# Kernel tuning notes

Hardware: AMD Instinct MI355X
Metric: run time of the kernel (lower is better)

Reference implementation:

```python
import jax, jax.numpy as jnp
from jax import lax
import numpy as np

B, T, H, NCLS = 64, 2048, 128, 4
CHANS = [1, 4, 8, 16, 96]


def setup_inputs() -> dict:
    key = jax.random.key(0)
    ks = iter(jax.random.split(key, 64))

    def n(shape, s=0.05):
        return jax.random.normal(next(ks), shape, jnp.float32) * s

    inp = {}
    inp["x"] = jax.random.normal(next(ks), (B, T, 1), jnp.float32)
    lengths = jnp.sort(jax.random.randint(next(ks), (B,), T // 2, T + 1))[::-1]
    inp["lengths"] = lengths.at[0].set(T).astype(jnp.int32)
    inp["ff_w"] = n((H, 1))
    inp["ff_b"] = n((H,))
    for l in range(2):
        din = H if l == 0 else 2 * H
        for d in ("f", "b"):
            inp[f"w_ih_l{l}{d}"] = n((4 * H, din))
            inp[f"w_hh_l{l}{d}"] = n((4 * H, H))
            inp[f"b_ih_l{l}{d}"] = n((4 * H,))
            inp[f"b_hh_l{l}{d}"] = n((4 * H,))
    for i in range(4):
        fan_in = CHANS[i] * 3
        inp[f"cw{i}"] = n((CHANS[i + 1], CHANS[i], 3), float(np.sqrt(2.0 / fan_in)))
        inp[f"cb{i}"] = n((CHANS[i + 1],))
    inp["lin_w"] = n((NCLS, 96 + 6 * H))
    inp["lin_b"] = n((NCLS,))
    return inp


def _lstm_scan(x, w_ih, w_hh, b_ih, b_hh):
    # x: [B, T, D] -> hidden states [B, T, H]; PyTorch gate order i,f,g,o
    b = x.shape[0]
    h0 = jnp.zeros((b, H), x.dtype)
    xg = jnp.swapaxes(x, 0, 1) @ w_ih.T + (b_ih + b_hh)  # [T, B, 4H] input contribution

    def step(carry, g_in):
        h, c = carry
        g = g_in + h @ w_hh.T
        i, f, gg, o = jnp.split(g, 4, axis=-1)
        c = jax.nn.sigmoid(f) * c + jax.nn.sigmoid(i) * jnp.tanh(gg)
        h = jax.nn.sigmoid(o) * jnp.tanh(c)
        return (h, c), h

    _, ys = lax.scan(step, (h0, h0), xg)
    return jnp.swapaxes(ys, 0, 1)


def _forward(x, lengths, ff_w, ff_b, lstm_params, conv_params, lin_w, lin_b):
    t = x.shape[1]
    mask = jnp.arange(t)[None, :] < lengths[:, None]            # [B, T]
    maskf = mask[..., None].astype(x.dtype)                      # [B, T, 1]
    # reversal index for packed-sequence-style backward direction (valid part reversed)
    rev_idx = jnp.clip(lengths[:, None] - 1 - jnp.arange(t)[None, :], 0, t - 1)[..., None]

    inp = (x @ ff_w.T + ff_b) * maskf                            # [B, T, H]
    for (wif, whf, bif, bhf, wib, whb, bib, bhb) in lstm_params:
        f_out = _lstm_scan(inp, wif, whf, bif, bhf)
        rin = jnp.take_along_axis(inp, rev_idx, axis=1) * maskf
        rys = _lstm_scan(rin, wib, whb, bib, bhb)
        b_out = jnp.take_along_axis(rys, rev_idx, axis=1)
        inp = jnp.concatenate([f_out, b_out], axis=-1) * maskf   # [B, T, 2H]

    rnn = inp
    lens = lengths.astype(x.dtype)[:, None]
    h_mean = (rnn * maskf).sum(1) / lens
    h_max = jnp.where(mask[..., None], rnn, -jnp.inf).max(1)
    h_last = jnp.take_along_axis(rnn, (lengths - 1)[:, None, None], axis=1)[:, 0]
    h = jnp.concatenate([h_mean, h_max, h_last], axis=1)         # [B, 6H]

    c = jnp.swapaxes(x, 1, 2)                                    # [B, 1, T]
    for cw, cb in conv_params:
        c = lax.conv_general_dilated(c, cw, (1,), 'VALID',
                                     dimension_numbers=('NCH', 'OIH', 'NCH'))
        c = jax.nn.relu(c + cb[None, :, None])
    cavg = c.mean(-1)                                            # [B, 96]

    out = jnp.concatenate([cavg, h], axis=1) @ lin_w.T + lin_b
    return out


def reference(x, lengths, ff_w, ff_b,
              w_ih_l0f, w_hh_l0f, b_ih_l0f, b_hh_l0f,
              w_ih_l0b, w_hh_l0b, b_ih_l0b, b_hh_l0b,
              w_ih_l1f, w_hh_l1f, b_ih_l1f, b_hh_l1f,
              w_ih_l1b, w_hh_l1b, b_ih_l1b, b_hh_l1b,
              cw0, cb0, cw1, cb1, cw2, cb2, cw3, cb3,
              lin_w, lin_b):
    lstm_params = [
        (w_ih_l0f, w_hh_l0f, b_ih_l0f, b_hh_l0f, w_ih_l0b, w_hh_l0b, b_ih_l0b, b_hh_l0b),
        (w_ih_l1f, w_hh_l1f, b_ih_l1f, b_hh_l1f, w_ih_l1b, w_hh_l1b, b_ih_l1b, b_hh_l1b),
    ]
    conv_params = [(cw0, cb0), (cw1, cb1), (cw2, cb2), (cw3, cb3)]
    return _forward(x, lengths, ff_w, ff_b, lstm_params, conv_params, lin_w, lin_b)
```

## Files before the change

### kernel.cpp

```cpp
#include <hip/hip_runtime.h>

using u16 = unsigned short;
using u32 = unsigned int;

typedef __attribute__((ext_vector_type(8))) short bf16x8;
typedef __attribute__((ext_vector_type(4))) float f32x4;

#define L2E 1.44269504f

__device__ __forceinline__ float bf2f(u16 u) {
  union { u32 i; float f; } v; v.i = ((u32)u) << 16; return v.f;
}
__device__ __forceinline__ u16 f2bf(float f) {
  union { float f; u32 i; } v; v.f = f;
  u32 i = v.i;
  return (u16)((i + 0x7FFFu + ((i >> 16) & 1u)) >> 16);
}
__device__ __forceinline__ float fexp2(float x) { float r; asm("v_exp_f32 %0, %1" : "=v"(r) : "v"(x)); return r; }
__device__ __forceinline__ float frcp(float x) { float r; asm("v_rcp_f32 %0, %1" : "=v"(r) : "v"(x)); return r; }
__device__ __forceinline__ float sig_s(float xp) { return frcp(1.0f + fexp2(-xp)); }
__device__ __forceinline__ float tanh_s(float x2) { return fmaf(-2.0f, frcp(1.0f + fexp2(x2)), 1.0f); }

__device__ __forceinline__ void barrier_lgkm() {
  asm volatile("s_waitcnt lgkmcnt(0)\n\ts_barrier" ::: "memory");
}

__device__ __forceinline__ float ldin(const void* p, long i, int f32) {
  return f32 ? ((const float*)p)[i] : bf2f(((const u16*)p)[i]);
}
__device__ __forceinline__ bf16x8 ldfrag(const void* p, long i, int f32) {
  if (!f32) return *(const bf16x8*)((const u16*)p + i);
  const float* f = (const float*)p + i;
  bf16x8 r;
#pragma unroll
  for (int j = 0; j < 8; ++j) r[j] = (short)f2bf(f[j]);
  return r;
}
__device__ __forceinline__ bf16x8 ldfrag_s(const void* p, long i, int f32, float s) {
  bf16x8 r;
  if (!f32) {
    const u16* h = (const u16*)p + i;
#pragma unroll
    for (int j = 0; j < 8; ++j) r[j] = (short)f2bf(bf2f(h[j]) * s);
  } else {
    const float* f = (const float*)p + i;
#pragma unroll
    for (int j = 0; j < 8; ++j) r[j] = (short)f2bf(f[j] * s);
  }
  return r;
}
__device__ __forceinline__ uint2 ld4(const void* p, long i, int f32) {
  if (!f32) return *(const uint2*)((const u16*)p + i);
  const float* f = (const float*)p + i;
  return make_uint2((u32)f2bf(f[0]) | ((u32)f2bf(f[1]) << 16),
                    (u32)f2bf(f[2]) | ((u32)f2bf(f[3]) << 16));
}

__device__ __forceinline__ int dtype_probe(const void* ffw) {
  const u16* h = (const u16*)ffw;
  int sane = 0;
  for (int i = 0; i < 64; ++i) {
    float v = bf2f(h[i]);
    sane += (v == v && fabsf(v) <= 1.0f) ? 1 : 0;
  }
  return (sane >= 60) ? 0 : 1;
}

__global__ void prep_k(const void* ffw, const void* ffb,
                       const void* wih0f, const void* bih0f, const void* bhh0f,
                       const void* wih0b, const void* bih0b, const void* bhh0b,
                       const void* bih1f, const void* bhh1f,
                       const void* bih1b, const void* bhh1b,
                       float* __restrict__ prep0, float* __restrict__ bias1) {
  const int f32 = dtype_probe(ffw);
  int dir = blockIdx.x, r = threadIdx.x;
  const void* wih  = dir ? wih0b : wih0f;
  const void* bih0 = dir ? bih0b : bih0f;
  const void* bhh0 = dir ? bhh0b : bhh0f;
  const void* bih1 = dir ? bih1b : bih1f;
  const void* bhh1 = dir ? bhh1b : bhh1f;
  float u = 0.f, v = 0.f;
  for (int k = 0; k < 128; ++k) {
    float wv = ldin(wih, r * 128 + k, f32);
    u += wv * ldin(ffw, k, f32);
    v += wv * ldin(ffb, k, f32);
  }
  const float sc = ((r >> 7) == 2) ? 2.0f * L2E : L2E;
  float bi = ldin(bih0, r, f32) + ldin(bhh0, r, f32);
  prep0[dir * 1536 + r]        = u * sc;
  prep0[dir * 1536 + 512 + r]  = (bi + v) * sc;
  prep0[dir * 1536 + 1024 + r] = bi * sc;
  bias1[dir * 512 + r] = (ldin(bih1, r, f32) + ldin(bhh1, r, f32)) * sc;
}

__device__ void conv_body(int blk, int tid, const void* x,
                          const void* cw0, const void* cb0, const void* cw1, const void* cb1,
                          const void* cw2, const void* cb2, const void* cw3, const void* cb3,
                          int f32, float* __restrict__ pcavg) {
  int b = blk >> 3, ck = blk & 7;
  int P = ck * 255;
  __shared__ float xs[264];
  __shared__ float c1s[4][264];
  __shared__ float c2s[8][264];
  __shared__ float w0s[12], w1s[96], w2s[384], w3s[4608];
  __shared__ float b0s[4], b1s[8], b2s[16], b3s[96];
  __shared__ float red[8][96];
  for (int i = tid; i < 263; i += 512) xs[i] = ldin(x, (long)b * 2048 + P + i, f32);
  for (int i = tid; i < 12; i += 512) w0s[i] = ldin(cw0, i, f32);
  for (int i = tid; i < 96; i += 512) w1s[i] = ldin(cw1, i, f32);
  for (int i = tid; i < 384; i += 512) w2s[i] = ldin(cw2, i, f32);
  for (int i = tid; i < 4608; i += 512) w3s[i] = ldin(cw3, i, f32);
  if (tid < 4) b0s[tid] = ldin(cb0, tid, f32);
  if (tid < 8) b1s[tid] = ldin(cb1, tid, f32);
  if (tid < 16) b2s[tid] = ldin(cb2, tid, f32);
  if (tid < 96) b3s[tid] = ldin(cb3, tid, f32);
  __syncthreads();
  for (int i = tid; i < 4 * 261; i += 512) {
    int ch = i / 261, t = i % 261;
    float s = b0s[ch];
#pragma unroll
    for (int d = 0; d < 3; ++d) s += w0s[ch * 3 + d] * xs[t + d];
    c1s[ch][t] = fmaxf(s, 0.f);
  }
  __syncthreads();
  for (int i = tid; i < 8 * 259; i += 512) {
    int ch = i / 259, t = i % 259;
    float s = b1s[ch];
    for (int ic = 0; ic < 4; ++ic)
#pragma unroll
      for (int d = 0; d < 3; ++d) s += w1s[(ch * 4 + ic) * 3 + d] * c1s[ic][t + d];
    c2s[ch][t] = fmaxf(s, 0.f);
  }
  __syncthreads();
  const bool act = tid < 255;
  float c3w[16][3];
#pragma unroll
  for (int m = 0; m < 16; ++m)
#pragma unroll
    for (int dt = 0; dt < 3; ++dt) c3w[m][dt] = 0.f;
  if (act) {
#pragma unroll
    for (int m = 0; m < 16; ++m)
#pragma unroll
      for (int dt = 0; dt < 3; ++dt) {
        float s = b2s[m];
        for (int ic = 0; ic < 8; ++ic)
#pragma unroll
          for (int d = 0; d < 3; ++d) s += w2s[(m * 8 + ic) * 3 + d] * c2s[ic][tid + dt + d];
        c3w[m][dt] = fmaxf(s, 0.f);
      }
  }
  int wv = tid >> 6, lane = tid & 63;
  for (int o = 0; o < 96; ++o) {
    float s = b3s[o];
#pragma unroll
    for (int m = 0; m < 16; ++m)
#pragma unroll
      for (int dt = 0; dt < 3; ++dt) s += w3s[(o * 16 + m) * 3 + dt] * c3w[m][dt];
    float v = act ? fmaxf(s, 0.f) : 0.f;
    for (int off = 32; off > 0; off >>= 1) v += __shfl_down(v, off, 64);
    if (lane == 0) red[wv][o] = v;
  }
  __syncthreads();
  if (tid < 96) {
    float s = 0.f;
#pragma unroll
    for (int k = 0; k < 8; ++k) s += red[k][tid];
    pcavg[(size_t)(b * 8 + ck) * 96 + tid] = s;
  }
}

__device__ void xg_gemm_body(int bi, int tid,
                             const void* wih1f, const void* wih1b,
                             const float* __restrict__ bias1,
                             const u16* __restrict__ f0, const u16* __restrict__ r0,
                             const int* __restrict__ lengths,
                             u16* __restrict__ xg_wr, int ct0, int tc, int f32) {
  const int TCB = 32;
  int nt = tc / TCB;
  int dir = bi / (4 * nt);
  int rem = bi % (4 * nt);
  int g = rem / nt, tcb = rem % nt;
  int tstart = ct0 + tcb * TCB;
  const int w = tid >> 6, lane = tid & 63, q = lane >> 4, col = lane & 15;

  const void* wih = dir ? wih1b : wih1f;
  bf16x8 af[4][8];
#pragma unroll
  for (int gt = 0; gt < 4; ++gt)
#pragma unroll
    for (int kt = 0; kt < 8; ++kt)
      af[gt][kt] = ldfrag(wih, (long)(gt * 128 + w * 16 + col) * 256 + kt * 32 + q * 8, f32);
  f32x4 bias4[4];
#pragma unroll
  for (int gt = 0; gt < 4; ++gt)
    bias4[gt] = *(const f32x4*)(bias1 + dir * 512 + gt * 128 + w * 16 + q * 4);

  __shared__ u16 bin[2][16][264];
  int sb = tid >> 5, sk = (tid & 31) * 8;
  int gb = g * 16 + sb;
  int len_s = lengths[gb];

  auto stage = [&](int t, int buf) {
    uint4 v = make_uint4(0u, 0u, 0u, 0u);
    if (t < len_s) {
      int qt = len_s - 1 - t; if (qt < 0) qt = 0;
      int th0 = dir ? qt : t;
      int th1 = dir ? t : qt;
      if (sk < 128)
        v = *(const uint4*)(f0 + ((size_t)th0 * 64 + gb) * 128 + sk);
      else
        v = *(const uint4*)(r0 + ((size_t)th1 * 64 + gb) * 128 + sk - 128);
    }
    *(uint4*)&bin[buf][sb][sk] = v;
  };
  stage(tstart, 0);
  const int bglob = g * 16 + col;
  const int G4o = bglob >> 2, c4g = bglob & 3;
  for (int i = 0; i < TCB; ++i) {
    int t = tstart + i, buf = i & 1;
    barrier_lgkm();
    if (i + 1 < TCB) stage(t + 1, buf ^ 1);
    bf16x8 bfr[8];
#pragma unroll
    for (int kt = 0; kt < 8; ++kt) bfr[kt] = *(const bf16x8*)(&bin[buf][col][kt * 32 + q * 8]);
    f32x4 acc[4];
#pragma unroll
    for (int gt = 0; gt < 4; ++gt) acc[gt] = (f32x4){0.f, 0.f, 0.f, 0.f};
#pragma unroll
    for (int kt = 0; kt < 8; ++kt)
#pragma unroll
      for (int gt = 0; gt < 4; ++gt)
        acc[gt] = __builtin_amdgcn_mfma_f32_16x16x32_bf16(af[gt][kt], bfr[kt], acc[gt], 0, 0, 0);
    size_t eb = ((((size_t)(t - ct0) * 2 + dir) * 16 + G4o) * 8 + w) * 256 + q * 64 + c4g * 4;
#pragma unroll
    for (int gt = 0; gt < 4; ++gt) {
      float sgt = (gt == 2) ? 2.0f * L2E : L2E;
#pragma unroll
      for (int r = 0; r < 4; ++r)
        xg_wr[eb + r * 16 + gt] = f2bf(fmaf(acc[gt][r], sgt, bias4[gt][r]));
    }
  }
}

__global__ __launch_bounds__(512, 2) void scan0_conv(
    const void* whhf, const void* whhb,
    const void* x, const float* __restrict__ prep0,
    const int* __restrict__ lengths,
    u16* __restrict__ outf, u16* __restrict__ outr,
    const void* cw0, const void* cb0, const void* cw1, const void* cb1,
    const void* cw2, const void* cb2, const void* cw3, const void* cb3,
    float* __restrict__ pcavg, const void* ffw) {
  const int f32 = dtype_probe(ffw);
  const int tid = threadIdx.x;
  if (blockIdx.x >= 32) {
    conv_body(blockIdx.x - 32, tid, x, cw0, cb0, cw1, cb1, cw2, cb2, cw3, cb3, f32, pcavg);
    return;
  }
  const int blk = blockIdx.x;
  const int dir = blk >> 4, G4 = blk & 15;
  const int w = tid >> 6, lane = tid & 63, q = lane >> 4, col = lane & 15;
  const int c4 = lane & 3, uu_ = lane >> 2;
  const int unit = w * 16 + uu_;
  const int b = G4 * 4 + c4;
  const bool jb1 = ((lane >> 2) & 1) != 0;
  const bool jb2 = ((lane >> 2) & 2) != 0;

  __shared__ u16 hbuf[2][4][160];
  __shared__ u16 xls[4 * 2056];

  const void* whh = dir ? whhb : whhf;
  bf16x8 afr[4][4];
#pragma unroll
  for (int gt = 0; gt < 4; ++gt) {
    float sgt = (gt == 2) ? 2.0f * L2E : L2E;
#pragma unroll
    for (int kt = 0; kt < 4; ++kt)
      afr[gt][kt] = ldfrag_s(whh, (long)(gt * 128 + w * 16 + col) * 128 + kt * 32 + q * 8, f32, sgt);
  }

  float uuc[4], ppc[4], bbc[4];
  {
    const float* pr = prep0 + dir * 1536;
#pragma unroll
    for (int gt = 0; gt < 4; ++gt) {
      int rb = gt * 128 + unit;
      uuc[gt] = pr[rb];
      ppc[gt] = pr[512 + rb];
      bbc[gt] = pr[1024 + rb];
    }
  }
  const int len_c = lengths[b];
  const int lm1 = dir ? (len_c - 1) : 0;
  const int sgn = dir ? -1 : 1;

  float cst = 0.f;
  hbuf[0][c4][unit] = 0; hbuf[1][c4][unit] = 0;
  for (int i = tid; i < 4 * 512; i += 512) {
    int row = i >> 9, t4 = (i & 511) * 4;
    *(uint2*)&xls[row * 2056 + t4] = ld4(x, (long)(G4 * 4 + row) * 2048 + t4, f32);
  }
  __syncthreads();

  auto mkpre = [&](int t, float* pre) {
    int tb = lm1 + sgn * t;
    tb = tb < 0 ? 0 : tb;
    float xv = bf2f(xls[c4 * 2056 + tb]);
    bool valid = t < len_c;
    float xvv = valid ? xv : 0.f;
#pragma unroll
    for (int gt = 0; gt < 4; ++gt)
      pre[gt] = fmaf(xvv, uuc[gt], valid ? ppc[gt] : bbc[gt]);
  };
  float pre[4];
  mkpre(0, pre);

  int p = 0;
  u16* outp = (dir ? outr : outf) + (size_t)b * 128 + unit;
  for (int t = 0; t < 2048; ++t) {
    bf16x8 bfr[4];
#pragma unroll
    for (int kt = 0; kt < 4; ++kt) bfr[kt] = *(const bf16x8*)(&hbuf[p][col & 3][kt * 32 + q * 8]);

    f32x4 acc[4];
#pragma unroll
    for (int gt = 0; gt < 4; ++gt) acc[gt] = (f32x4){0.f, 0.f, 0.f, 0.f};
#pragma unroll
    for (int kt = 0; kt < 4; ++kt)
#pragma unroll
      for (int gt = 0; gt < 4; ++gt)
        acc[gt] = __builtin_amdgcn_mfma_f32_16x16x32_bf16(afr[gt][kt], bfr[kt], acc[gt], 0, 0, 0);

    float gv[4];
#pragma unroll
    for (int gt = 0; gt < 4; ++gt) {
      float a = jb2 ? acc[gt][2] : acc[gt][0];
      float c = jb2 ? acc[gt][3] : acc[gt][1];
      gv[gt] = (jb1 ? c : a) + pre[gt];
    }

    float sf = sig_s(gv[1]);
    float si = sig_s(gv[0]);
    float tg = tanh_s(gv[2]);
    float so = sig_s(gv[3]);
    float cs = fmaf(sf, cst, si * tg);
    cst = cs;
    float hv = so * tanh_s(cs * (2.0f * L2E));
    u16 hb = f2bf(hv);
    hbuf[p ^ 1][c4][unit] = hb;
    *outp = hb;
    outp += 8192;
    mkpre(t + 1, pre);
    barrier_lgkm();
    p ^= 1;
  }
}

__global__ __launch_bounds__(512, 2) void scan1_gemm(
    const void* whhf, const void* whhb,
    const u16* __restrict__ xg_rd, u16* __restrict__ xg_wr,
    const void* wih1f, const void* wih1b, const float* __restrict__ bias1,
    const u16* __restrict__ f0, const u16* __restrict__ r0,
    const int* __restrict__ lengths,
    float* __restrict__ cstate, u16* __restrict__ hstate,
    float* __restrict__ pacc, float* __restrict__ hfeat,
    const void* ffw, int t0, int t1, int gct0, int TCc) {
  const int f32 = dtype_probe(ffw);
  const int tid = threadIdx.x;
  if (blockIdx.x >= 32) {
    xg_gemm_body(blockIdx.x - 32, tid, wih1f, wih1b, bias1, f0, r0, lengths,
                 xg_wr, gct0, TCc, f32);
    return;
  }
  const int blk = blockIdx.x;
  const int dir = blk >> 4, G4 = blk & 15;
  const int w = tid >> 6, lane = tid & 63, q = lane >> 4, col = lane & 15;
  const int c4 = lane & 3, uu_ = lane >> 2;
  const int unit = w * 16 + uu_;
  const int b = G4 * 4 + c4;
  const bool jb1 = ((lane >> 2) & 1) != 0;
  const bool jb2 = ((lane >> 2) & 2) != 0;

  __shared__ u16 hbuf[2][4][160];

  const void* whh = dir ? whhb : whhf;
  bf16x8 afr[4][4];
#pragma unroll
  for (int gt = 0; gt < 4; ++gt) {
    float sgt = (gt == 2) ? 2.0f * L2E : L2E;
#pragma unroll
    for (int kt = 0; kt < 4; ++kt)
      afr[gt][kt] = ldfrag_s(whh, (long)(gt * 128 + w * 16 + col) * 128 + kt * 32 + q * 8, f32, sgt);
  }
  const int len_c = lengths[b];
  const int lastt = dir ? 0 : (len_c - 1);

  int p = t0 & 1;
  float cst, psum, pmax, plast;
  if (t0 == 0) {
    cst = 0.f;
    hbuf[0][c4][unit] = 0; hbuf[1][c4][unit] = 0;
    psum = 0.f; pmax = -1e30f; plast = 0.f;
  } else {
    cst = cstate[blk * 512 + tid];
    hbuf[p][c4][unit] = hstate[blk * 512 + c4 * 128 + unit];
    long pb = (long)(blk * 512 + tid) * 4;
    psum = pacc[pb]; pmax = pacc[pb + 1]; plast = pacc[pb + 2];
  }
  __syncthreads();

  const u16* xgp = xg_rd + (((size_t)dir * 16 + G4) * 8 + w) * 256 + (size_t)lane * 4;
  float xf[4];
  auto unpack = [&](uint2 c, float* o) {
    o[0] = bf2f((u16)(c.x & 0xffffu));
    o[1] = bf2f((u16)(c.x >> 16));
    o[2] = bf2f((u16)(c.y & 0xffffu));
    o[3] = bf2f((u16)(c.y >> 16));
  };
  uint2 nxtA, nxtB;
  {
    uint2 c0 = *(const uint2*)xgp;
    unpack(c0, xf);
    nxtA = (t0 + 1 < t1) ? *(const uint2*)(xgp + 65536) : make_uint2(0, 0);
    nxtB = (t0 + 2 < t1) ? *(const uint2*)(xgp + 2 * 65536) : make_uint2(0, 0);
    xgp += (size_t)3 * 65536;
  }

  for (int t = t0; t < t1; ++t) {
    bf16x8 bfr[4];
#pragma unroll
    for (int kt = 0; kt < 4; ++kt) bfr[kt] = *(const bf16x8*)(&hbuf[p][col & 3][kt * 32 + q * 8]);

    f32x4 acc[4];
#pragma unroll
    for (int gt = 0; gt < 4; ++gt) acc[gt] = (f32x4){0.f, 0.f, 0.f, 0.f};
#pragma unroll
    for (int kt = 0; kt < 4; ++kt)
#pragma unroll
      for (int gt = 0; gt < 4; ++gt)
        acc[gt] = __builtin_amdgcn_mfma_f32_16x16x32_bf16(afr[gt][kt], bfr[kt], acc[gt], 0, 0, 0);

    float gv[4];
#pragma unroll
    for (int gt = 0; gt < 4; ++gt) {
      float a = jb2 ? acc[gt][2] : acc[gt][0];
      float c = jb2 ? acc[gt][3] : acc[gt][1];
      gv[gt] = (jb1 ? c : a) + xf[gt];
    }

    float sf = sig_s(gv[1]);
    float si = sig_s(gv[0]);
    float tg = tanh_s(gv[2]);
    float so = sig_s(gv[3]);
    float cs = fmaf(sf, cst, si * tg);
    cst = cs;
    float hv = so * tanh_s(cs * (2.0f * L2E));
    u16 hb = f2bf(hv);
    hbuf[p ^ 1][c4][unit] = hb;
    bool inlen = t < len_c;
    psum += inlen ? hv : 0.f;
    pmax = fmaxf(pmax, inlen ? hv : -1e30f);
    plast = (t == lastt) ? hv : plast;
    unpack(nxtA, xf);
    nxtA = nxtB;
    if (t + 3 < t1) nxtB = *(const uint2*)xgp;
    xgp += 65536;
    barrier_lgkm();
    p ^= 1;
  }

  cstate[blk * 512 + tid] = cst;
  hstate[blk * 512 + c4 * 128 + unit] = hbuf[p][c4][unit];
  {
    long pb = (long)(blk * 512 + tid) * 4;
    pacc[pb] = psum; pacc[pb + 1] = pmax; pacc[pb + 2] = plast;
  }
  if (t1 == 2048) {
    int base = b * 768 + dir * 128 + unit;
    hfeat[base]       = psum / (float)len_c;
    hfeat[base + 256] = pmax;
    hfeat[base + 512] = plast;
  }
}

__global__ __launch_bounds__(512, 2) void xg_gemm0(
    const void* wih1f, const void* wih1b, const float* __restrict__ bias1,
    const u16* __restrict__ f0, const u16* __restrict__ r0,
    const int* __restrict__ lengths,
    u16* __restrict__ xg_wr, const void* ffw, int ct0, int tc) {
  xg_gemm_body(blockIdx.x, threadIdx.x, wih1f, wih1b, bias1, f0, r0, lengths,
               xg_wr, ct0, tc, dtype_probe(ffw));
}

__global__ void final_k(const float* __restrict__ pcavg, const float* __restrict__ hfeat,
                        const void* lw, const void* lb,
                        const void* ffw, void* outv) {
  const int f32 = dtype_probe(ffw);
  int b = blockIdx.x, tid = threadIdx.x;
  float p0 = 0.f, p1 = 0.f, p2 = 0.f, p3 = 0.f;
  for (int k = tid; k < 864; k += 64) {
    float f;
    if (k < 96) {
      float s = 0.f;
#pragma unroll
      for (int c = 0; c < 8; ++c) s += pcavg[(size_t)(b * 8 + c) * 96 + k];
      f = s / 2040.f;
    } else {
      f = hfeat[b * 768 + k - 96];
    }
    p0 += f * ldin(lw, k, f32);
    p1 += f * ldin(lw, 864 + k, f32);
    p2 += f * ldin(lw, 2 * 864 + k, f32);
    p3 += f * ldin(lw, 3 * 864 + k, f32);
  }
  for (int off = 32; off > 0; off >>= 1) {
    p0 += __shfl_down(p0, off, 64);
    p1 += __shfl_down(p1, off, 64);
    p2 += __shfl_down(p2, off, 64);
    p3 += __shfl_down(p3, off, 64);
  }
  if (tid == 0) {
    float v0 = p0 + ldin(lb, 0, f32), v1 = p1 + ldin(lb, 1, f32);
    float v2 = p2 + ldin(lb, 2, f32), v3 = p3 + ldin(lb, 3, f32);
    if (f32) {
      float* o = (float*)outv;
      o[b * 4 + 0] = v0; o[b * 4 + 1] = v1; o[b * 4 + 2] = v2; o[b * 4 + 3] = v3;
    } else {
      u16* o = (u16*)outv;
      o[b * 4 + 0] = f2bf(v0); o[b * 4 + 1] = f2bf(v1);
      o[b * 4 + 2] = f2bf(v2); o[b * 4 + 3] = f2bf(v3);
    }
  }
}

extern "C" void kernel_launch(void* const* d_in, const int* in_sizes, int n_in,
                              void* d_out, int out_size, void* d_ws, size_t ws_size,
                              hipStream_t stream) {
  const void* x      = d_in[0];
  const int* lengths = (const int*)d_in[1];
  const void* ffw = d_in[2];
  const void* ffb = d_in[3];
  const void* wih0f = d_in[4];  const void* whh0f = d_in[5];
  const void* bih0f = d_in[6];  const void* bhh0f = d_in[7];
  const void* wih0b = d_in[8];  const void* whh0b = d_in[9];
  const void* bih0b = d_in[10]; const void* bhh0b = d_in[11];
  const void* wih1f = d_in[12]; const void* whh1f = d_in[13];
  const void* bih1f = d_in[14]; const void* bhh1f = d_in[15];
  const void* wih1b = d_in[16]; const void* whh1b = d_in[17];
  const void* bih1b = d_in[18]; const void* bhh1b = d_in[19];
  const void* cw0 = d_in[20]; const void* cb0 = d_in[21];
  const void* cw1 = d_in[22]; const void* cb1 = d_in[23];
  const void* cw2 = d_in[24]; const void* cb2 = d_in[25];
  const void* cw3 = d_in[26]; const void* cb3 = d_in[27];
  const void* lw = d_in[28];  const void* lb = d_in[29];

  float* prep0  = (float*)d_ws + 16;
  float* bias1  = prep0 + 3072;
  float* pcavg  = bias1 + 1024;
  float* hfeat  = pcavg + 49152;
  float* cstate = hfeat + 49152;
  float* pacc   = cstate + 16384;
  u16* f0 = (u16*)(pacc + 65536);
  const size_t SEQ = (size_t)2048 * 64 * 128;
  u16* r0 = f0 + SEQ;
  u16* hstate = r0 + SEQ;
  u16* xg = hstate + 16384;

  size_t base_bytes = (size_t)((char*)xg - (char*)d_ws);
  int TC = 32;
  for (int cand = 512; cand >= 32; cand >>= 1)
    if (ws_size >= base_bytes + (size_t)2 * cand * 65536 * 2) { TC = cand; break; }

  prep_k<<<2, 512, 0, stream>>>(ffw, ffb, wih0f, bih0f, bhh0f, wih0b, bih0b, bhh0b,
                                bih1f, bhh1f, bih1b, bhh1b, prep0, bias1);
  scan0_conv<<<544, 512, 0, stream>>>(whh0f, whh0b, x, prep0, lengths, f0, r0,
                                      cw0, cb0, cw1, cb1, cw2, cb2, cw3, cb3,
                                      pcavg, ffw);
  const int nch = 2048 / TC;
  xg_gemm0<<<TC / 4, 512, 0, stream>>>(wih1f, wih1b, bias1, f0, r0, lengths,
                                       xg, ffw, 0, TC);
  for (int ch = 0; ch < nch; ++ch) {
    u16* xg_rd = xg + (size_t)(ch & 1) * TC * 65536;
    u16* xg_wr = xg + (size_t)((ch + 1) & 1) * TC * 65536;
    int gblocks = (ch + 1 < nch) ? TC / 4 : 0;
    scan1_gemm<<<32 + gblocks, 512, 0, stream>>>(
        whh1f, whh1b, xg_rd, xg_wr, wih1f, wih1b, bias1, f0, r0, lengths,
        cstate, hstate, pacc, hfeat, ffw, ch * TC, (ch + 1) * TC, (ch + 1) * TC, TC);
  }
  final_k<<<64, 64, 0, stream>>>(pcavg, hfeat, lw, lb, ffw, d_out);
}
```

Baseline: 2.438 ms.

## Pack two logical 512-thread blocks into each 1024-thread workgroup

Each 1024-thread workgroup now runs two independent virtual blocks (seq = tid>>9), each with its own copy of the shared-memory arrays. Grid sizes are halved for the scan, conv and xg-gemm kernels, and launch bounds change to (1024,1). The aim appears to be co-locating the two recurrent scan streams on one CU, or changing scheduling, for the latency-bound LSTM scans. The cost is that __syncthreads and the barriers now span both halves, coupling their progress. Register budget under the (1024,1) bound may also be tighter.

```diff
diff --git a/kernel.cpp b/kernel.cpp
--- a/kernel.cpp
+++ b/kernel.cpp
@@ -93,43 +93,43 @@
   bias1[dir * 512 + r] = (ldin(bih1, r, f32) + ldin(bhh1, r, f32)) * sc;
 }
 
-__device__ void conv_body(int blk, int tid, const void* x,
+__device__ void conv_body(int blk, int s, int tid, const void* x,
                           const void* cw0, const void* cb0, const void* cw1, const void* cb1,
                           const void* cw2, const void* cb2, const void* cw3, const void* cb3,
                           int f32, float* __restrict__ pcavg) {
   int b = blk >> 3, ck = blk & 7;
   int P = ck * 255;
-  __shared__ float xs[264];
-  __shared__ float c1s[4][264];
-  __shared__ float c2s[8][264];
-  __shared__ float w0s[12], w1s[96], w2s[384], w3s[4608];
-  __shared__ float b0s[4], b1s[8], b2s[16], b3s[96];
-  __shared__ float red[8][96];
-  for (int i = tid; i < 263; i += 512) xs[i] = ldin(x, (long)b * 2048 + P + i, f32);
-  for (int i = tid; i < 12; i += 512) w0s[i] = ldin(cw0, i, f32);
-  for (int i = tid; i < 96; i += 512) w1s[i] = ldin(cw1, i, f32);
-  for (int i = tid; i < 384; i += 512) w2s[i] = ldin(cw2, i, f32);
-  for (int i = tid; i < 4608; i += 512) w3s[i] = ldin(cw3, i, f32);
-  if (tid < 4) b0s[tid] = ldin(cb0, tid, f32);
-  if (tid < 8) b1s[tid] = ldin(cb1, tid, f32);
-  if (tid < 16) b2s[tid] = ldin(cb2, tid, f32);
-  if (tid < 96) b3s[tid] = ldin(cb3, tid, f32);
+  __shared__ float xs[2][264];
+  __shared__ float c1s[2][4][264];
+  __shared__ float c2s[2][8][264];
+  __shared__ float w0s[2][12], w1s[2][96], w2s[2][384], w3s[2][4608];
+  __shared__ float b0s[2][4], b1s[2][8], b2s[2][16], b3s[2][96];
+  __shared__ float red[2][8][96];
+  for (int i = tid; i < 263; i += 512) xs[s][i] = ldin(x, (long)b * 2048 + P + i, f32);
+  for (int i = tid; i < 12; i += 512) w0s[s][i] = ldin(cw0, i, f32);
+  for (int i = tid; i < 96; i += 512) w1s[s][i] = ldin(cw1, i, f32);
+  for (int i = tid; i < 384; i += 512) w2s[s][i] = ldin(cw2, i, f32);
+  for (int i = tid; i < 4608; i += 512) w3s[s][i] = ldin(cw3, i, f32);
+  if (tid < 4) b0s[s][tid] = ldin(cb0, tid, f32);
+  if (tid < 8) b1s[s][tid] = ldin(cb1, tid, f32);
+  if (tid < 16) b2s[s][tid] = ldin(cb2, tid, f32);
+  if (tid < 96) b3s[s][tid] = ldin(cb3, tid, f32);
   __syncthreads();
   for (int i = tid; i < 4 * 261; i += 512) {
     int ch = i / 261, t = i % 261;
-    float s = b0s[ch];
-#pragma unroll
-    for (int d = 0; d < 3; ++d) s += w0s[ch * 3 + d] * xs[t + d];
-    c1s[ch][t] = fmaxf(s, 0.f);
+    float v = b0s[s][ch];
+#pragma unroll
+    for (int d = 0; d < 3; ++d) v += w0s[s][ch * 3 + d] * xs[s][t + d];
+    c1s[s][ch][t] = fmaxf(v, 0.f);
   }
   __syncthreads();
   for (int i = tid; i < 8 * 259; i += 512) {
     int ch = i / 259, t = i % 259;
-    float s = b1s[ch];
+    float v = b1s[s][ch];
     for (int ic = 0; ic < 4; ++ic)
 #pragma unroll
-      for (int d = 0; d < 3; ++d) s += w1s[(ch * 4 + ic) * 3 + d] * c1s[ic][t + d];
-    c2s[ch][t] = fmaxf(s, 0.f);
+      for (int d = 0; d < 3; ++d) v += w1s[s][(ch * 4 + ic) * 3 + d] * c1s[s][ic][t + d];
+    c2s[s][ch][t] = fmaxf(v, 0.f);
   }
   __syncthreads();
   const bool act = tid < 255;
@@ -143,34 +143,34 @@
     for (int m = 0; m < 16; ++m)
 #pragma unroll
       for (int dt = 0; dt < 3; ++dt) {
-        float s = b2s[m];
+        float v = b2s[s][m];
         for (int ic = 0; ic < 8; ++ic)
 #pragma unroll
-          for (int d = 0; d < 3; ++d) s += w2s[(m * 8 + ic) * 3 + d] * c2s[ic][tid + dt + d];
-        c3w[m][dt] = fmaxf(s, 0.f);
+          for (int d = 0; d < 3; ++d) v += w2s[s][(m * 8 + ic) * 3 + d] * c2s[s][ic][tid + dt + d];
+        c3w[m][dt] = fmaxf(v, 0.f);
       }
   }
   int wv = tid >> 6, lane = tid & 63;
   for (int o = 0; o < 96; ++o) {
-    float s = b3s[o];
+    float v = b3s[s][o];
 #pragma unroll
     for (int m = 0; m < 16; ++m)
 #pragma unroll
-      for (int dt = 0; dt < 3; ++dt) s += w3s[(o * 16 + m) * 3 + dt] * c3w[m][dt];
-    float v = act ? fmaxf(s, 0.f) : 0.f;
-    for (int off = 32; off > 0; off >>= 1) v += __shfl_down(v, off, 64);
-    if (lane == 0) red[wv][o] = v;
+      for (int dt = 0; dt < 3; ++dt) v += w3s[s][(o * 16 + m) * 3 + dt] * c3w[m][dt];
+    float vr = act ? fmaxf(v, 0.f) : 0.f;
+    for (int off = 32; off > 0; off >>= 1) vr += __shfl_down(vr, off, 64);
+    if (lane == 0) red[s][wv][o] = vr;
   }
   __syncthreads();
   if (tid < 96) {
-    float s = 0.f;
-#pragma unroll
-    for (int k = 0; k < 8; ++k) s += red[k][tid];
-    pcavg[(size_t)(b * 8 + ck) * 96 + tid] = s;
-  }
-}
-
-__device__ void xg_gemm_body(int bi, int tid,
+    float v = 0.f;
+#pragma unroll
+    for (int k = 0; k < 8; ++k) v += red[s][k][tid];
+    pcavg[(size_t)(b * 8 + ck) * 96 + tid] = v;
+  }
+}
+
+__device__ void xg_gemm_body(int bi, int s, int tid,
                              const void* wih1f, const void* wih1b,
                              const float* __restrict__ bias1,
                              const u16* __restrict__ f0, const u16* __restrict__ r0,
@@ -196,7 +196,7 @@
   for (int gt = 0; gt < 4; ++gt)
     bias4[gt] = *(const f32x4*)(bias1 + dir * 512 + gt * 128 + w * 16 + q * 4);
 
-  __shared__ u16 bin[2][16][264];
+  __shared__ u16 bin[2][2][16][264];
   int sb = tid >> 5, sk = (tid & 31) * 8;
   int gb = g * 16 + sb;
   int len_s = lengths[gb];
@@ -212,7 +212,7 @@
       else
         v = *(const uint4*)(r0 + ((size_t)th1 * 64 + gb) * 128 + sk - 128);
     }
-    *(uint4*)&bin[buf][sb][sk] = v;
+    *(uint4*)&bin[s][buf][sb][sk] = v;
   };
   stage(tstart, 0);
   const int bglob = g * 16 + col;
@@ -223,7 +223,7 @@
     if (i + 1 < TCB) stage(t + 1, buf ^ 1);
     bf16x8 bfr[8];
 #pragma unroll
-    for (int kt = 0; kt < 8; ++kt) bfr[kt] = *(const bf16x8*)(&bin[buf][col][kt * 32 + q * 8]);
+    for (int kt = 0; kt < 8; ++kt) bfr[kt] = *(const bf16x8*)(&bin[s][buf][col][kt * 32 + q * 8]);
     f32x4 acc[4];
 #pragma unroll
     for (int gt = 0; gt < 4; ++gt) acc[gt] = (f32x4){0.f, 0.f, 0.f, 0.f};
@@ -243,7 +243,7 @@
   }
 }
 
-__global__ __launch_bounds__(512, 2) void scan0_conv(
+__global__ __launch_bounds__(1024, 1) void scan0_conv(
     const void* whhf, const void* whhb,
     const void* x, const float* __restrict__ prep0,
     const int* __restrict__ lengths,
@@ -253,21 +253,23 @@
     float* __restrict__ pcavg, const void* ffw) {
   const int f32 = dtype_probe(ffw);
   const int tid = threadIdx.x;
-  if (blockIdx.x >= 32) {
-    conv_body(blockIdx.x - 32, tid, x, cw0, cb0, cw1, cb1, cw2, cb2, cw3, cb3, f32, pcavg);
+  const int seq = tid >> 9, vtid = tid & 511;
+  if (blockIdx.x >= 16) {
+    conv_body((blockIdx.x - 16) * 2 + seq, seq, vtid,
+              x, cw0, cb0, cw1, cb1, cw2, cb2, cw3, cb3, f32, pcavg);
     return;
   }
-  const int blk = blockIdx.x;
-  const int dir = blk >> 4, G4 = blk & 15;
-  const int w = tid >> 6, lane = tid & 63, q = lane >> 4, col = lane & 15;
+  const int vblk = blockIdx.x * 2 + seq;
+  const int dir = vblk >> 4, G4 = vblk & 15;
+  const int w = vtid >> 6, lane = vtid & 63, q = lane >> 4, col = lane & 15;
   const int c4 = lane & 3, uu_ = lane >> 2;
   const int unit = w * 16 + uu_;
   const int b = G4 * 4 + c4;
   const bool jb1 = ((lane >> 2) & 1) != 0;
   const bool jb2 = ((lane >> 2) & 2) != 0;
 
-  __shared__ u16 hbuf[2][4][160];
-  __shared__ u16 xls[4 * 2056];
+  __shared__ u16 hbuf[2][2][4][160];
+  __shared__ u16 xls[2][4 * 2056];
 
   const void* whh = dir ? whhb : whhf;
   bf16x8 afr[4][4];
@@ -295,17 +297,18 @@
   const int sgn = dir ? -1 : 1;
 
   float cst = 0.f;
-  hbuf[0][c4][unit] = 0; hbuf[1][c4][unit] = 0;
-  for (int i = tid; i < 4 * 512; i += 512) {
+  hbuf[seq][0][c4][unit] = 0; hbuf[seq][1][c4][unit] = 0;
+  for (int i = vtid; i < 4 * 512; i += 512) {
     int row = i >> 9, t4 = (i & 511) * 4;
-    *(uint2*)&xls[row * 2056 + t4] = ld4(x, (long)(G4 * 4 + row) * 2048 + t4, f32);
+    *(uint2*)&xls[seq][row * 2056 + t4] = ld4(x, (long)(G4 * 4 + row) * 2048 + t4, f32);
   }
   __syncthreads();
 
+  const u16* xbase = &xls[seq][c4 * 2056];
   auto mkpre = [&](int t, float* pre) {
     int tb = lm1 + sgn * t;
     tb = tb < 0 ? 0 : tb;
-    float xv = bf2f(xls[c4 * 2056 + tb]);
+    float xv = bf2f(xbase[tb]);
     bool valid = t < len_c;
     float xvv = valid ? xv : 0.f;
 #pragma unroll
@@ -320,7 +323,7 @@
   for (int t = 0; t < 2048; ++t) {
     bf16x8 bfr[4];
 #pragma unroll
-    for (int kt = 0; kt < 4; ++kt) bfr[kt] = *(const bf16x8*)(&hbuf[p][col & 3][kt * 32 + q * 8]);
+    for (int kt = 0; kt < 4; ++kt) bfr[kt] = *(const bf16x8*)(&hbuf[seq][p][col & 3][kt * 32 + q * 8]);
 
     f32x4 acc[4];
 #pragma unroll
@@ -347,7 +350,7 @@
     cst = cs;
     float hv = so * tanh_s(cs * (2.0f * L2E));
     u16 hb = f2bf(hv);
-    hbuf[p ^ 1][c4][unit] = hb;
+    hbuf[seq][p ^ 1][c4][unit] = hb;
     *outp = hb;
     outp += 8192;
     mkpre(t + 1, pre);
@@ -356,7 +359,7 @@
   }
 }
 
-__global__ __launch_bounds__(512, 2) void scan1_gemm(
+__global__ __launch_bounds__(1024, 1) void scan1_gemm(
     const void* whhf, const void* whhb,
     const u16* __restrict__ xg_rd, u16* __restrict__ xg_wr,
     const void* wih1f, const void* wih1b, const float* __restrict__ bias1,
@@ -367,21 +370,22 @@
     const void* ffw, int t0, int t1, int gct0, int TCc) {
   const int f32 = dtype_probe(ffw);
   const int tid = threadIdx.x;
-  if (blockIdx.x >= 32) {
-    xg_gemm_body(blockIdx.x - 32, tid, wih1f, wih1b, bias1, f0, r0, lengths,
-                 xg_wr, gct0, TCc, f32);
+  const int seq = tid >> 9, vtid = tid & 511;
+  if (blockIdx.x >= 16) {
+    xg_gemm_body((blockIdx.x - 16) * 2 + seq, seq, vtid,
+                 wih1f, wih1b, bias1, f0, r0, lengths, xg_wr, gct0, TCc, f32);
     return;
   }
-  const int blk = blockIdx.x;
-  const int dir = blk >> 4, G4 = blk & 15;
-  const int w = tid >> 6, lane = tid & 63, q = lane >> 4, col = lane & 15;
+  const int vblk = blockIdx.x * 2 + seq;
+  const int dir = vblk >> 4, G4 = vblk & 15;
+  const int w = vtid >> 6, lane = vtid & 63, q = lane >> 4, col = lane & 15;
   const int c4 = lane & 3, uu_ = lane >> 2;
   const int unit = w * 16 + uu_;
   const int b = G4 * 4 + c4;
   const bool jb1 = ((lane >> 2) & 1) != 0;
   const bool jb2 = ((lane >> 2) & 2) != 0;
 
-  __shared__ u16 hbuf[2][4][160];
+  __shared__ u16 hbuf[2][2][4][160];
 
   const void* whh = dir ? whhb : whhf;
   bf16x8 afr[4][4];
@@ -399,12 +403,12 @@
   float cst, psum, pmax, plast;
   if (t0 == 0) {
     cst = 0.f;
-    hbuf[0][c4][unit] = 0; hbuf[1][c4][unit] = 0;
+    hbuf[seq][0][c4][unit] = 0; hbuf[seq][1][c4][unit] = 0;
     psum = 0.f; pmax = -1e30f; plast = 0.f;
   } else {
-    cst = cstate[blk * 512 + tid];
-    hbuf[p][c4][unit] = hstate[blk * 512 + c4 * 128 + unit];
-    long pb = (long)(blk * 512 + tid) * 4;
+    cst = cstate[vblk * 512 + vtid];
+    hbuf[seq][p][c4][unit] = hstate[vblk * 512 + c4 * 128 + unit];
+    long pb = (long)(vblk * 512 + vtid) * 4;
     psum = pacc[pb]; pmax = pacc[pb + 1]; plast = pacc[pb + 2];
   }
   __syncthreads();
@@ -429,7 +433,7 @@
   for (int t = t0; t < t1; ++t) {
     bf16x8 bfr[4];
 #pragma unroll
-    for (int kt = 0; kt < 4; ++kt) bfr[kt] = *(const bf16x8*)(&hbuf[p][col & 3][kt * 32 + q * 8]);
+    for (int kt = 0; kt < 4; ++kt) bfr[kt] = *(const bf16x8*)(&hbuf[seq][p][col & 3][kt * 32 + q * 8]);
 
     f32x4 acc[4];
 #pragma unroll
@@ -456,7 +460,7 @@
     cst = cs;
     float hv = so * tanh_s(cs * (2.0f * L2E));
     u16 hb = f2bf(hv);
-    hbuf[p ^ 1][c4][unit] = hb;
+    hbuf[seq][p ^ 1][c4][unit] = hb;
     bool inlen = t < len_c;
     psum += inlen ? hv : 0.f;
     pmax = fmaxf(pmax, inlen ? hv : -1e30f);
@@ -469,10 +473,10 @@
     p ^= 1;
   }
 
-  cstate[blk * 512 + tid] = cst;
-  hstate[blk * 512 + c4 * 128 + unit] = hbuf[p][c4][unit];
+  cstate[vblk * 512 + vtid] = cst;
+  hstate[vblk * 512 + c4 * 128 + unit] = hbuf[seq][p][c4][unit];
   {
-    long pb = (long)(blk * 512 + tid) * 4;
+    long pb = (long)(vblk * 512 + vtid) * 4;
     pacc[pb] = psum; pacc[pb + 1] = pmax; pacc[pb + 2] = plast;
   }
   if (t1 == 2048) {
@@ -483,13 +487,14 @@
   }
 }
 
-__global__ __launch_bounds__(512, 2) void xg_gemm0(
+__global__ __launch_bounds__(1024, 1) void xg_gemm0(
     const void* wih1f, const void* wih1b, const float* __restrict__ bias1,
     const u16* __restrict__ f0, const u16* __restrict__ r0,
     const int* __restrict__ lengths,
     u16* __restrict__ xg_wr, const void* ffw, int ct0, int tc) {
-  xg_gemm_body(blockIdx.x, threadIdx.x, wih1f, wih1b, bias1, f0, r0, lengths,
-               xg_wr, ct0, tc, dtype_probe(ffw));
+  const int tid = threadIdx.x;
+  xg_gemm_body(blockIdx.x * 2 + (tid >> 9), tid >> 9, tid & 511,
+               wih1f, wih1b, bias1, f0, r0, lengths, xg_wr, ct0, tc, dtype_probe(ffw));
 }
 
 __global__ void final_k(const float* __restrict__ pcavg, const float* __restrict__ hfeat,
@@ -573,17 +578,17 @@
 
   prep_k<<<2, 512, 0, stream>>>(ffw, ffb, wih0f, bih0f, bhh0f, wih0b, bih0b, bhh0b,
                                 bih1f, bhh1f, bih1b, bhh1b, prep0, bias1);
-  scan0_conv<<<544, 512, 0, stream>>>(whh0f, whh0b, x, prep0, lengths, f0, r0,
-                                      cw0, cb0, cw1, cb1, cw2, cb2, cw3, cb3,
-                                      pcavg, ffw);
+  scan0_conv<<<16 + 256, 1024, 0, stream>>>(whh0f, whh0b, x, prep0, lengths, f0, r0,
+                                            cw0, cb0, cw1, cb1, cw2, cb2, cw3, cb3,
+                                            pcavg, ffw);
   const int nch = 2048 / TC;
-  xg_gemm0<<<TC / 4, 512, 0, stream>>>(wih1f, wih1b, bias1, f0, r0, lengths,
-                                       xg, ffw, 0, TC);
+  xg_gemm0<<<TC / 8, 1024, 0, stream>>>(wih1f, wih1b, bias1, f0, r0, lengths,
+                                        xg, ffw, 0, TC);
   for (int ch = 0; ch < nch; ++ch) {
     u16* xg_rd = xg + (size_t)(ch & 1) * TC * 65536;
     u16* xg_wr = xg + (size_t)((ch + 1) & 1) * TC * 65536;
-    int gblocks = (ch + 1 < nch) ? TC / 4 : 0;
-    scan1_gemm<<<32 + gblocks, 512, 0, stream>>>(
+    int gblocks = (ch + 1 < nch) ? TC / 8 : 0;
+    scan1_gemm<<<16 + gblocks, 1024, 0, stream>>>(
         whh1f, whh1b, xg_rd, xg_wr, wih1f, wih1b, bias1, f0, r0, lengths,
         cstate, hstate, pacc, hfeat, ffw, ch * TC, (ch + 1) * TC, (ch + 1) * TC, TC);
   }
```

New measurement: 4.267 ms. 1.75x slower.
